# Kernel optimization log

Hardware: AMD Instinct MI355X
Metric: run time of the kernel (lower is better)

The kernel has to match this reference:

```python
import jax, jax.numpy as jnp
import numpy as np

K = 2          # kernel_size
NQ = 4         # n_qubits = K*K
NL = 2         # n_layers


def setup_inputs() -> dict:
    key = jax.random.key(0)
    ks = jax.random.split(key, 6)
    x = jax.random.uniform(ks[0], (64, 1, 128, 128), jnp.float32, 0.0, np.pi)
    conv_w = jax.random.normal(ks[1], (1, 1, K, K), jnp.float32) * 0.5
    conv_b = jax.random.normal(ks[2], (1,), jnp.float32) * 0.1
    ry_angles = jax.random.normal(ks[3], (NL, NQ), jnp.float32)  # fixed RY params
    head_w = jax.random.normal(ks[4], (1, 2), jnp.float32) * 0.5
    head_b = jax.random.normal(ks[5], (1,), jnp.float32) * 0.1
    return {"x": x, "conv_w": conv_w, "conv_b": conv_b,
            "ry_angles": ry_angles, "head_w": head_w, "head_b": head_b}


def _rx(state, theta, wire):
    # state: (N, 2,2,2,2) complex; theta: (N,) batched angle
    ax = wire + 1
    st = jnp.moveaxis(state, ax, 1)
    s0, s1 = st[:, 0], st[:, 1]                      # (N, 2,2,2)
    c = jnp.cos(theta * 0.5).reshape((-1, 1, 1, 1))
    s = jnp.sin(theta * 0.5).reshape((-1, 1, 1, 1))
    n0 = c * s0 - 1j * s * s1
    n1 = -1j * s * s0 + c * s1
    return jnp.moveaxis(jnp.stack([n0, n1], axis=1), 1, ax)


def _ry(state, phi, wire):
    # phi: scalar shared angle
    ax = wire + 1
    st = jnp.moveaxis(state, ax, 1)
    s0, s1 = st[:, 0], st[:, 1]
    c = jnp.cos(phi * 0.5)
    s = jnp.sin(phi * 0.5)
    n0 = c * s0 - s * s1
    n1 = s * s0 + c * s1
    return jnp.moveaxis(jnp.stack([n0, n1], axis=1), 1, ax)


def _cnot(state, ctrl, tgt):
    ca, ta = ctrl + 1, tgt + 1
    st = jnp.moveaxis(state, (ca, ta), (1, 2))       # (N, 2, 2, rest)
    new = jnp.stack([st[:, 0], st[:, 1, ::-1]], axis=1)  # flip target where ctrl=1
    return jnp.moveaxis(new, (1, 2), (ca, ta))


def _quantum_expval_z0(patch_flat, ry_angles):
    # patch_flat: (N, 4) -> expval PauliZ(wire 0), shape (N,)
    N = patch_flat.shape[0]
    state = jnp.zeros((N, 2, 2, 2, 2), jnp.complex64).at[:, 0, 0, 0, 0].set(1.0)
    for w in range(NQ):
        state = _rx(state, patch_flat[:, w], w)
    for l in range(NL):
        for w in range(NQ):
            state = _ry(state, ry_angles[l, w], w)
        for w in range(0, NQ - 1, 2):
            state = _cnot(state, w, w + 1)
    p = jnp.real(state) ** 2 + jnp.imag(state) ** 2   # (N,2,2,2,2)
    return p[:, 0].sum(axis=(1, 2, 3)) - p[:, 1].sum(axis=(1, 2, 3))


def reference(x, conv_w, conv_b, ry_angles, head_w, head_b):
    B, _, H, W = x.shape
    # all KxK sliding patches, feature order (c, kh, kw) row-major == patch.view(-1)
    patches = jax.lax.conv_general_dilated_patches(x, (K, K), (1, 1), 'VALID')  # (B,4,Ph,Pw)
    Ph, Pw = patches.shape[2], patches.shape[3]
    pf = patches.transpose(0, 2, 3, 1).reshape(-1, K * K)   # (N, 4)
    conv_out = pf @ conv_w.reshape(K * K) + conv_b[0]       # (N,)
    q_out = _quantum_expval_z0(pf, ry_angles)               # (N,)
    per_patch = head_w[0, 0] * conv_out + head_w[0, 1] * q_out + head_b[0]
    out = per_patch.reshape(B, Ph * Pw).mean(axis=1)        # mean over windows
    return out[:, None]
```

## Files before the change

### kernel.cpp

```cpp
#include <hip/hip_runtime.h>
#include <math.h>


#define XW 128
#define NP (127 * 127)
#define NB 64
#define NBLK 16
#define BLK 256

__device__ __forceinline__ void circuit_coeffs(const float* __restrict__ ry,
                                               float k[5]) {
    float U[4][4] = {{1,0,0,0},{0,1,0,0},{0,0,1,0},{0,0,0,1}};
    for (int l = 0; l < 2; ++l) {
        float s0, c0, s1, c1;
        __sincosf(0.5f * ry[l*4+0], &s0, &c0);
        __sincosf(0.5f * ry[l*4+1], &s1, &c1);
        for (int q1 = 0; q1 < 2; ++q1)
            for (int c = 0; c < 4; ++c) {
                float a = U[q1][c], d = U[2+q1][c];
                U[q1][c]   = c0*a - s0*d;
                U[2+q1][c] = s0*a + c0*d;
            }
        for (int m = 0; m < 2; ++m)
            for (int c = 0; c < 4; ++c) {
                float a = U[2*m][c], d = U[2*m+1][c];
                U[2*m][c]   = c1*a - s1*d;
                U[2*m+1][c] = s1*a + c1*d;
            }
        for (int c = 0; c < 4; ++c) { float t = U[2][c]; U[2][c] = U[3][c]; U[3][c] = t; }
    }
    float pA=0, pB=0, pC=0, pD=0, pAD=0, pBC=0;
    for (int r = 0; r < 4; ++r) {
        float g = (r < 2) ? 1.f : -1.f;
        pA  += g * U[r][0] * U[r][0];
        pB  += g * U[r][1] * U[r][1];
        pC  += g * U[r][2] * U[r][2];
        pD  += g * U[r][3] * U[r][3];
        pAD += g * U[r][0] * U[r][3];
        pBC += g * U[r][1] * U[r][2];
    }
    k[0] = 0.25f * (pA + pB + pC + pD);
    k[1] = 0.25f * (pA + pB - pC - pD);
    k[2] = 0.25f * (pA - pB + pC - pD);
    k[3] = 0.25f * (pA - pB - pC + pD);
    k[4] = 0.50f * (pBC - pAD);
}

__global__ __launch_bounds__(BLK) void row_kernel(
    const float* __restrict__ x,
    const float* __restrict__ conv_w,
    const float* __restrict__ head_w,
    const float* __restrict__ ry,
    float* __restrict__ part)
{
    __shared__ float sk[4];
    __shared__ float red[BLK / 64];

    const int tid  = threadIdx.x;
    const int lane = tid & 63;
    const int wave = tid >> 6;
    const int half = lane >> 5;
    const int col0 = (lane & 31) << 2;
    const int img  = blockIdx.y;
    const int row  = (blockIdx.x << 3) + (wave << 1) + half;

    if (tid == 0) {
        float k[5];
        circuit_coeffs(ry, k);
        const float hw1 = head_w[1];
        sk[0] = hw1 * k[1]; sk[1] = hw1 * k[2];
        sk[2] = hw1 * k[3]; sk[3] = hw1 * k[4];
    }
    __syncthreads();

    const float hw0 = head_w[0];
    const float w0 = hw0 * conv_w[0], w1 = hw0 * conv_w[1];
    const float w2 = hw0 * conv_w[2], w3 = hw0 * conv_w[3];
    const float k1 = sk[0], k2 = sk[1], k3 = sk[2], k4 = sk[3];

    const float P = (row < 127 ? w0 : 0.f) + (row > 0 ? w2 : 0.f);
    const float Q = (row < 127 ? w1 : 0.f) + (row > 0 ? w3 : 0.f);
    const float PQ = P + Q;

    const float4 e = ((const float4*)(x + ((size_t)img * 128 + row) * XW))
                         [lane & 31];

    float acc = e.x * (col0 == 0 ? P : PQ)
              + e.y * PQ
              + e.z * PQ
              + e.w * (col0 == 124 ? Q : PQ);

    if (row < 127) {
        float s0,c0,s1,c1,s2,c2,s3,c3;
        __sincosf(e.x, &s0, &c0);
        __sincosf(e.y, &s1, &c1);
        __sincosf(e.z, &s2, &c2);
        __sincosf(e.w, &s3, &c3);
        const float cn = __shfl_down(c0, 1, 64);
        const float sn = __shfl_down(s0, 1, 64);
        acc += k1 * c0 + k2 * c1 + k3 * c0 * c1 + k4 * s0 * s1;
        acc += k1 * c1 + k2 * c2 + k3 * c1 * c2 + k4 * s1 * s2;
        acc += k1 * c2 + k2 * c3 + k3 * c2 * c3 + k4 * s2 * s3;
        if (col0 < 124)
            acc += k1 * c3 + k2 * cn + k3 * c3 * cn + k4 * s3 * sn;
    }

    for (int off = 32; off > 0; off >>= 1)
        acc += __shfl_down(acc, off, 64);
    if (lane == 0) red[wave] = acc;
    __syncthreads();
    if (tid == 0)
        part[img * NBLK + blockIdx.x] = red[0] + red[1] + red[2] + red[3];
}

__global__ __launch_bounds__(64) void final_kernel(
    const float* __restrict__ part,
    const float* __restrict__ conv_b,
    const float* __restrict__ ry,
    const float* __restrict__ head_w,
    const float* __restrict__ head_b,
    float* __restrict__ out)
{
    const int b = threadIdx.x;
    float k[5];
    circuit_coeffs(ry, k);
    float sum = 0.f;
    for (int s = 0; s < NBLK; ++s) sum += part[b * NBLK + s];
    const float cconst = head_w[0] * conv_b[0] + head_w[1] * k[0] + head_b[0];
    out[b] = sum * (1.0f / NP) + cconst;
}

extern "C" void kernel_launch(void* const* d_in, const int* in_sizes, int n_in,
                              void* d_out, int out_size, void* d_ws, size_t ws_size,
                              hipStream_t stream) {
    const float* x      = (const float*)d_in[0];
    const float* conv_w = (const float*)d_in[1];
    const float* conv_b = (const float*)d_in[2];
    const float* ry     = (const float*)d_in[3];
    const float* head_w = (const float*)d_in[4];
    const float* head_b = (const float*)d_in[5];
    float* out  = (float*)d_out;
    float* part = (float*)d_ws;

    dim3 grid(NBLK, NB);
    row_kernel<<<grid, BLK, 0, stream>>>(x, conv_w, head_w, ry, part);
    final_kernel<<<1, 64, 0, stream>>>(part, conv_b, ry, head_w, head_b, out);
}
```

Measured before the change: 65.43 us.

## Fuse row and final kernels into one block-per-image kernel

Replaces the two-kernel scheme (1024 row blocks writing partials plus a single-block final reduction) with one kernel launching a 1024-thread block per image, each thread processing four float4 loads over the image. The in-block reduction writes the final mean directly, which removes the second launch and the workspace round trip. The trade-off is only 64 blocks on a GPU with many more CUs, so parallelism and latency hiding drop considerably.

```diff
diff --git a/kernel.cpp b/kernel.cpp
--- a/kernel.cpp
+++ b/kernel.cpp
@@ -2,11 +2,10 @@
 #include <math.h>
 
 
-#define XW 128
 #define NP (127 * 127)
 #define NB 64
-#define NBLK 16
-#define BLK 256
+#define BLK 1024
+#define PASSES 4
 
 __device__ __forceinline__ void circuit_coeffs(const float* __restrict__ ry,
                                                float k[5]) {
@@ -46,12 +45,14 @@
     k[4] = 0.50f * (pBC - pAD);
 }
 
-__global__ __launch_bounds__(BLK) void row_kernel(
+__global__ __launch_bounds__(BLK) void image_kernel(
     const float* __restrict__ x,
     const float* __restrict__ conv_w,
+    const float* __restrict__ conv_b,
+    const float* __restrict__ ry,
     const float* __restrict__ head_w,
-    const float* __restrict__ ry,
-    float* __restrict__ part)
+    const float* __restrict__ head_b,
+    float* __restrict__ out)
 {
     __shared__ float sk[4];
     __shared__ float red[BLK / 64];
@@ -59,17 +60,17 @@
     const int tid  = threadIdx.x;
     const int lane = tid & 63;
     const int wave = tid >> 6;
-    const int half = lane >> 5;
-    const int col0 = (lane & 31) << 2;
-    const int img  = blockIdx.y;
-    const int row  = (blockIdx.x << 3) + (wave << 1) + half;
+    const int img  = blockIdx.x;
+    const int col0 = (tid & 31) << 2;
 
+    float cconst = 0.f;
     if (tid == 0) {
         float k[5];
         circuit_coeffs(ry, k);
         const float hw1 = head_w[1];
         sk[0] = hw1 * k[1]; sk[1] = hw1 * k[2];
         sk[2] = hw1 * k[3]; sk[3] = hw1 * k[4];
+        cconst = head_w[0] * conv_b[0] + hw1 * k[0] + head_b[0];
     }
     __syncthreads();
 
@@ -78,19 +79,24 @@
     const float w2 = hw0 * conv_w[2], w3 = hw0 * conv_w[3];
     const float k1 = sk[0], k2 = sk[1], k3 = sk[2], k4 = sk[3];
 
-    const float P = (row < 127 ? w0 : 0.f) + (row > 0 ? w2 : 0.f);
-    const float Q = (row < 127 ? w1 : 0.f) + (row > 0 ? w3 : 0.f);
-    const float PQ = P + Q;
+    const float4* __restrict__ xi = (const float4*)(x + (size_t)img * 16384);
 
-    const float4 e = ((const float4*)(x + ((size_t)img * 128 + row) * XW))
-                         [lane & 31];
+    float acc = 0.f;
+#pragma unroll
+    for (int p = 0; p < PASSES; ++p) {
+        const int idx = p * BLK + tid;
+        const int row = idx >> 5;
+        const float4 e = xi[idx];
 
-    float acc = e.x * (col0 == 0 ? P : PQ)
-              + e.y * PQ
-              + e.z * PQ
-              + e.w * (col0 == 124 ? Q : PQ);
+        const float P = (row < 127 ? w0 : 0.f) + (row > 0 ? w2 : 0.f);
+        const float Q = (row < 127 ? w1 : 0.f) + (row > 0 ? w3 : 0.f);
+        const float PQ = P + Q;
 
-    if (row < 127) {
+        acc += e.x * (col0 == 0 ? P : PQ)
+             + e.y * PQ
+             + e.z * PQ
+             + e.w * (col0 == 124 ? Q : PQ);
+
         float s0,c0,s1,c1,s2,c2,s3,c3;
         __sincosf(e.x, &s0, &c0);
         __sincosf(e.y, &s1, &c1);
@@ -98,36 +104,26 @@
         __sincosf(e.w, &s3, &c3);
         const float cn = __shfl_down(c0, 1, 64);
         const float sn = __shfl_down(s0, 1, 64);
-        acc += k1 * c0 + k2 * c1 + k3 * c0 * c1 + k4 * s0 * s1;
-        acc += k1 * c1 + k2 * c2 + k3 * c1 * c2 + k4 * s1 * s2;
-        acc += k1 * c2 + k2 * c3 + k3 * c2 * c3 + k4 * s2 * s3;
-        if (col0 < 124)
-            acc += k1 * c3 + k2 * cn + k3 * c3 * cn + k4 * s3 * sn;
+        if (row < 127) {
+            acc += k1 * c0 + k2 * c1 + k3 * c0 * c1 + k4 * s0 * s1;
+            acc += k1 * c1 + k2 * c2 + k3 * c1 * c2 + k4 * s1 * s2;
+            acc += k1 * c2 + k2 * c3 + k3 * c2 * c3 + k4 * s2 * s3;
+            if (col0 < 124)
+                acc += k1 * c3 + k2 * cn + k3 * c3 * cn + k4 * s3 * sn;
+        }
     }
 
     for (int off = 32; off > 0; off >>= 1)
         acc += __shfl_down(acc, off, 64);
     if (lane == 0) red[wave] = acc;
     __syncthreads();
-    if (tid == 0)
-        part[img * NBLK + blockIdx.x] = red[0] + red[1] + red[2] + red[3];
-}
-
-__global__ __launch_bounds__(64) void final_kernel(
-    const float* __restrict__ part,
-    const float* __restrict__ conv_b,
-    const float* __restrict__ ry,
-    const float* __restrict__ head_w,
-    const float* __restrict__ head_b,
-    float* __restrict__ out)
-{
-    const int b = threadIdx.x;
-    float k[5];
-    circuit_coeffs(ry, k);
-    float sum = 0.f;
-    for (int s = 0; s < NBLK; ++s) sum += part[b * NBLK + s];
-    const float cconst = head_w[0] * conv_b[0] + head_w[1] * k[0] + head_b[0];
-    out[b] = sum * (1.0f / NP) + cconst;
+    if (wave == 0) {
+        float v = (lane < BLK / 64) ? red[lane] : 0.f;
+        for (int off = 8; off > 0; off >>= 1)
+            v += __shfl_down(v, off, 64);
+        if (tid == 0)
+            out[img] = v * (1.0f / NP) + cconst;
+    }
 }
 
 extern "C" void kernel_launch(void* const* d_in, const int* in_sizes, int n_in,
@@ -139,10 +135,8 @@
     const float* ry     = (const float*)d_in[3];
     const float* head_w = (const float*)d_in[4];
     const float* head_b = (const float*)d_in[5];
-    float* out  = (float*)d_out;
-    float* part = (float*)d_ws;
+    float* out = (float*)d_out;
 
-    dim3 grid(NBLK, NB);
-    row_kernel<<<grid, BLK, 0, stream>>>(x, conv_w, head_w, ry, part);
-    final_kernel<<<1, 64, 0, stream>>>(part, conv_b, ry, head_w, head_b, out);
+    image_kernel<<<NB, BLK, 0, stream>>>(x, conv_w, conv_b, ry, head_w,
+                                         head_b, out);
 }
```

New measurement: 66.15 us. Within noise of the previous version (+1.1%).
